# Kernel optimization log

Measured on AMD Instinct MI355X. Metric: run time of the kernel, lower is better.

## Reference

```python
import jax, jax.numpy as jnp
import numpy as np
from jax import lax

B, G, D, S = 1, 2048, 64, 2
H_FULL = 200
H0 = H_FULL // 2 ** (S - 1)
PC_RANGE = (-50.0, -50.0, -4.0, 50.0, 50.0, 4.0)
THRESH = 0.05
CHUNK = 128


def conv3x3(x, w):
    # x: [b,c,h,w], w: [o,i,3,3]
    return lax.conv_general_dilated(x, w, (1, 1), 'SAME',
                                    dimension_numbers=('NCHW', 'OIHW', 'NCHW'))


def instance_norm(x, eps=1e-5):
    mu = x.mean(axis=(2, 3), keepdims=True)
    var = x.var(axis=(2, 3), keepdims=True)
    return (x - mu) / jnp.sqrt(var + eps)


def basic_block(x, w1, w2):
    # conv-(BN@init=identity)-relu-conv-(BN)-add-relu
    h = jax.nn.relu(conv3x3(x, w1))
    h = conv3x3(h, w2)
    return jax.nn.relu(x + h)


def upsampling_add(x, skip, w):
    b, c, h, wd = x.shape
    xu = jax.image.resize(x, (b, c, 2 * h, 2 * wd), method='bilinear')
    xu = instance_norm(conv3x3(xu, w))
    return xu + skip


def render_stage(means, cov6, feats, opac, mask, H, W):
    # Orthographic BEV splatting (3DGS-style EWA + front-to-back compositing).
    g, d = feats.shape
    sh = H / 100.0
    sw = W / 100.0
    # full_proj_transform: px = -sh*y + H/2 ; py = -sw*x + W/2
    u = -sh * means[:, 1] + 0.5 * H
    v = -sw * means[:, 0] + 0.5 * W
    # cov2d = J Sigma J^T + 0.3*I, J = [[0,-sh,0],[-sw,0,0]]
    a = sh * sh * cov6[:, 3] + 0.3
    c = sw * sw * cov6[:, 0] + 0.3
    bb = sh * sw * cov6[:, 1]
    det = jnp.maximum(a * c - bb * bb, 1e-8)
    A = c / det
    Bc = -bb / det
    C = a / det
    xs = jnp.arange(W, dtype=jnp.float32)
    ys = jnp.arange(H, dtype=jnp.float32)
    nc = g // CHUNK

    def step(carry, inp):
        T, out = carry
        u_, v_, A_, B_, C_, op_, mk_, ft_ = inp
        dx = u_[:, None, None] - xs[None, None, :]
        dy = v_[:, None, None] - ys[None, :, None]
        power = (-0.5 * (A_[:, None, None] * dx * dx + C_[:, None, None] * dy * dy)
                 - B_[:, None, None] * dx * dy)
        alpha = jnp.minimum(op_[:, None, None] * jnp.exp(power), 0.99)
        alpha = jnp.where((alpha >= 1.0 / 255.0) & mk_[:, None, None] & (power <= 0.0),
                          alpha, 0.0)
        cp = jnp.cumprod(1.0 - alpha, axis=0)
        t_exc = jnp.concatenate([jnp.ones_like(cp[:1]), cp[:-1]], 0) * T
        out = out + jnp.einsum('ghw,gd->dhw', alpha * t_exc, ft_)
        return (T * cp[-1], out), None

    ch = lambda arr: arr.reshape(nc, CHUNK, *arr.shape[1:])
    init = (jnp.ones((H, W), jnp.float32), jnp.zeros((d, H, W), jnp.float32))
    (_, out), _ = lax.scan(step, init,
                           (ch(u), ch(v), ch(A), ch(Bc), ch(C), ch(opac), ch(mask), ch(feats)))
    return out  # bg color = 0


def setup_inputs() -> dict:
    key = jax.random.key(0)
    ks = jax.random.split(key, 10)
    features = jax.random.normal(ks[0], (B, G, D), jnp.float32)
    xy = jax.random.uniform(ks[1], (B, G, 2), jnp.float32, -55.0, 55.0)
    z = jax.random.uniform(ks[2], (B, G, 1), jnp.float32, -5.0, 5.0)
    means3D = jnp.concatenate([xy, z], -1)
    L = jax.random.normal(ks[3], (B, G, 3, 3), jnp.float32) * 0.5
    Sig = jnp.einsum('bgij,bgkj->bgik', L, L) + 0.1 * jnp.eye(3, dtype=jnp.float32)
    cov3D = jnp.stack([Sig[..., 0, 0], Sig[..., 0, 1], Sig[..., 0, 2],
                       Sig[..., 1, 1], Sig[..., 1, 2], Sig[..., 2, 2]], -1)
    opacities = jax.random.uniform(ks[4], (B, G, S), jnp.float32)
    w_scale = 1.0 / np.sqrt(D * 9)
    bev_emb = jax.random.normal(ks[5], (H0 * H0, D), jnp.float32) * 0.02
    conv1_w = jax.random.normal(ks[6], (S, D, D, 3, 3), jnp.float32) * w_scale
    blk_w = jax.random.normal(ks[7], (S, 2, 2, D, D, 3, 3), jnp.float32) * w_scale
    up_w = jax.random.normal(ks[8], (S - 1, D, D, 3, 3), jnp.float32) * w_scale
    return {'features': features, 'means3D': means3D, 'cov3D': cov3D,
            'opacities': opacities, 'bev_emb': bev_emb, 'conv1_w': conv1_w,
            'blk_w': blk_w, 'up_w': up_w}


def reference(features, means3D, cov3D, opacities, bev_emb, conv1_w, blk_w, up_w):
    b = features.shape[0]
    d = features.shape[-1]
    m = means3D
    mask_pos = ((m[..., 0] >= PC_RANGE[0]) & (m[..., 0] <= PC_RANGE[3]) &
                (m[..., 1] >= PC_RANGE[1]) & (m[..., 1] <= PC_RANGE[4]) &
                (m[..., 2] >= PC_RANGE[2]) & (m[..., 2] <= PC_RANGE[5]))
    num_g = jnp.float32(0.0)
    bevs = []
    for s in range(S):
        H = H0 * 2 ** s
        mask = (opacities[..., s] > THRESH) & mask_pos
        rend = jax.vmap(lambda mn, cv, ft, op, mk: render_stage(mn, cv, ft, op, mk, H, H))
        bevs.append(rend(means3D, cov3D, features, opacities[..., s], mask))
        num_g = num_g + jnp.mean(jnp.sum(mask.astype(jnp.float32), 1))
    x = jnp.broadcast_to(jnp.transpose(bev_emb.reshape(H0, H0, d), (2, 0, 1))[None],
                         (b, d, H0, H0))
    for s in range(S):
        bev = conv3x3(bevs[s], conv1_w[s])
        if s == 0:
            x = x + bev
        else:
            x = upsampling_add(x, bev, up_w[s - 1])
        for blk in range(2):
            x = basic_block(x, blk_w[s, blk, 0], blk_w[s, blk, 1])
    return x, num_g
```

## Files before the change

### kernel.cpp

```cpp
#include <hip/hip_runtime.h>
#include <math.h>

#define G_N 2048
#define CCH 256
#define PSTR 12
#define NBLK 1024
#define WC (64 * 64 * 9)

typedef short bhalf8 __attribute__((ext_vector_type(8)));
typedef float f32x4 __attribute__((ext_vector_type(4)));
typedef unsigned short u16;

__device__ __forceinline__ u16 f2bf(float f) {
    unsigned u = __float_as_uint(f);
    unsigned r = (u + 0x7fffu + ((u >> 16) & 1u)) >> 16;
    return (u16)r;
}
__device__ __forceinline__ float b2f(u16 h) {
    return __uint_as_float((unsigned)h << 16);
}

__device__ __forceinline__ ushort4 chload4(const u16* p) {
    unsigned long long u = __hip_atomic_load((const unsigned long long*)p,
        __ATOMIC_RELAXED, __HIP_MEMORY_SCOPE_AGENT);
    union { unsigned long long u; ushort4 s; } x; x.u = u;
    return x.s;
}
__device__ __forceinline__ void chstore4(u16* p, ushort4 v) {
    union { unsigned long long u; ushort4 s; } x; x.s = v;
    __hip_atomic_store((unsigned long long*)p, x.u,
                       __ATOMIC_RELAXED, __HIP_MEMORY_SCOPE_AGENT);
}
__device__ __forceinline__ float cload(const float* p) {
    return __hip_atomic_load(p, __ATOMIC_RELAXED, __HIP_MEMORY_SCOPE_AGENT);
}

__device__ __forceinline__ void gbar(int* leaf, int* root, int* flag, int phase) {
    asm volatile("s_waitcnt vmcnt(0) lgkmcnt(0)" ::: "memory");
    __syncthreads();
    if (threadIdx.x == 0) {
        int g = blockIdx.x >> 5;
        int old = atomicAdd(&leaf[g * 16], 1);
        if ((old & 31) == 31) {
            int o2 = atomicAdd(root, 1);
            if ((o2 & 31) == 31)
                __hip_atomic_store(flag, phase, __ATOMIC_RELAXED,
                                   __HIP_MEMORY_SCOPE_AGENT);
        }
        while (__hip_atomic_load(flag, __ATOMIC_RELAXED,
                                 __HIP_MEMORY_SCOPE_AGENT) < phase)
            __builtin_amdgcn_s_sleep(4);
    }
    __syncthreads();
    asm volatile("" ::: "memory");
}

__global__ void gls_init(const float* __restrict__ conv1_w,
                         const float* __restrict__ blk_w,
                         const float* __restrict__ up_w,
                         u16* __restrict__ wprep,
                         const float* __restrict__ means,
                         const float* __restrict__ cov6,
                         const float* __restrict__ opac,
                         float* __restrict__ params,
                         int* __restrict__ counts,
                         int* __restrict__ barmem,
                         float* __restrict__ sacc)
{
    int bx = blockIdx.x;
    int tid = threadIdx.x;
    if (bx == 200) {
        for (int i = tid; i < 520; i += 256) barmem[i] = 0;
        if (tid < 128) sacc[tid] = 0.f;
        return;
    }
    if (bx < 198) {
        int p = bx % 18, c = bx / 18;
        const float* src;
        if (c == 0) src = conv1_w;
        else if (c <= 4) src = blk_w + (c - 1) * WC;
        else if (c == 5) src = conv1_w + WC;
        else if (c == 6) src = up_w;
        else src = blk_w + (c - 3) * WC;
        int tap = p >> 1;
        int m = tid >> 6, lane = tid & 63;
        int oc = m * 16 + (lane & 15);
        int ci0 = (p & 1) * 32 + (lane >> 4) * 8;
        u16 v[8];
#pragma unroll
        for (int j = 0; j < 8; ++j)
            v[j] = f2bf(src[(oc * 64 + ci0 + j) * 9 + tap]);
        u16* dst = wprep + ((c * 18 + p) * 4 + m) * 64 * 8 + lane * 8;
#pragma unroll
        for (int j = 0; j < 8; ++j) dst[j] = v[j];
        return;
    }
    int s = bx - 198;
    __shared__ int s_base;
    __shared__ int s_wsum[4];
    if (tid == 0) s_base = 0;
    __syncthreads();
    float* P = params + s * G_N * PSTR;
    float H = (float)(100 << s);
    float sh = (float)(1 << s);
    for (int it = 0; it < G_N / 256; ++it) {
        int g = it * 256 + tid;
        float mx = means[g * 3 + 0], my = means[g * 3 + 1], mz = means[g * 3 + 2];
        float op = opac[g * 2 + s];
        bool mask = (mx >= -50.f && mx <= 50.f && my >= -50.f && my <= 50.f &&
                     mz >= -4.f && mz <= 4.f && op > 0.05f);
        unsigned long long bal = __ballot(mask);
        int lane = tid & 63, wid = tid >> 6;
        int prefix = __popcll(bal & ((1ull << lane) - 1ull));
        if (lane == 0) s_wsum[wid] = __popcll(bal);
        __syncthreads();
        int woff = 0;
        for (int w = 0; w < 4; ++w) if (w < wid) woff += s_wsum[w];
        int pos = s_base + woff + prefix;
        if (mask) {
            float u = -sh * my + 0.5f * H;
            float v = -sh * mx + 0.5f * H;
            float a = sh * sh * cov6[g * 6 + 3] + 0.3f;
            float c = sh * sh * cov6[g * 6 + 0] + 0.3f;
            float bb = sh * sh * cov6[g * 6 + 1];
            float det = fmaxf(a * c - bb * bb, 1e-8f);
            float t = logf(255.f * op);
            float* Q = P + pos * PSTR;
            Q[0] = u; Q[1] = v;
            Q[2] = c / det; Q[3] = -bb / det; Q[4] = a / det;
            Q[5] = op; Q[6] = -t;
            Q[7] = __int_as_float(g);
            Q[8] = sqrtf(2.f * t * a);
            Q[9] = sqrtf(2.f * t * c);
            Q[10] = 0.f; Q[11] = 0.f;
        }
        __syncthreads();
        if (tid == 0) s_base += s_wsum[0] + s_wsum[1] + s_wsum[2] + s_wsum[3];
        __syncthreads();
    }
    if (tid == 0) counts[s] = s_base;
}

__device__ __forceinline__ void render_tile(
    int unit, const float* __restrict__ params, const int* __restrict__ counts,
    const float* __restrict__ feats, u16* __restrict__ out0,
    u16* __restrict__ out1, char* smem)
{
    int s = (unit < 49) ? 0 : 1;
    int t = (s == 0) ? unit : unit - 49;
    int tw = (s == 0) ? 7 : 13;
    int bxx = t % tw, byy = t / tw;
    int H = 100 << s;
    const float* P = params + s * G_N * PSTR;
    u16* out = s ? out1 : out0;
    int cnt = counts[s];

    float* raw = (float*)smem;
    float* cmp = raw + CCH * PSTR;
    int* s_wsum = (int*)(smem + 24576);

    int tid = threadIdx.x;
    int txl = tid & 15, tyl = tid >> 4;
    int px = bxx * 16 + txl;
    int py = byy * 16 + tyl;
    bool active = (px < H) && (py < H);
    float fx = (float)px, fy = (float)py;
    float tx0 = (float)(bxx * 16);
    float tx1 = (float)min(H - 1, bxx * 16 + 15);
    float ty0 = (float)(byy * 16);
    float ty1 = (float)min(H - 1, byy * 16 + 15);

    f32x4 acc[16];
#pragma unroll
    for (int k = 0; k < 16; ++k) acc[k] = (f32x4){0.f, 0.f, 0.f, 0.f};
    float T = 1.f;

    for (int base = 0; base < cnt; base += CCH) {
        int anyalive = __syncthreads_or((int)(active && T > 1e-6f));
        if (!anyalive) break;
        int n = min(CCH, cnt - base);
        for (int i = tid; i < n * 3; i += 256)
            ((float4*)raw)[i] = ((const float4*)(P + base * PSTR))[i];
        __syncthreads();
        bool pass = false;
        if (tid < n) {
            float u = raw[tid * PSTR + 0], v = raw[tid * PSTR + 1];
            float rx = raw[tid * PSTR + 8], ry = raw[tid * PSTR + 9];
            pass = (u + rx >= tx0) && (u - rx <= tx1) &&
                   (v + ry >= ty0) && (v - ry <= ty1);
        }
        unsigned long long bal = __ballot(pass);
        int lane = tid & 63, wid = tid >> 6;
        int prefix = __popcll(bal & ((1ull << lane) - 1ull));
        if (lane == 0) s_wsum[wid] = __popcll(bal);
        __syncthreads();
        int woff = 0;
        for (int w = 0; w < 4; ++w) if (w < wid) woff += s_wsum[w];
        if (pass) {
            float4* dst = (float4*)(cmp + (woff + prefix) * PSTR);
            const float4* src = (const float4*)(raw + tid * PSTR);
            dst[0] = src[0]; dst[1] = src[1]; dst[2] = src[2];
        }
        __syncthreads();
        int nc = s_wsum[0] + s_wsum[1] + s_wsum[2] + s_wsum[3];
        if (active && T > 1e-6f) {
            for (int j = 0; j < nc; ++j) {
                float4 q0 = *(const float4*)(cmp + j * PSTR);
                float4 q1 = *(const float4*)(cmp + j * PSTR + 4);
                float dx = q0.x - fx, dy = q0.y - fy;
                float power = -0.5f * (q0.z * dx * dx + q1.x * dy * dy) - q0.w * dx * dy;
                if (power <= 0.f && power >= q1.z) {
                    float alpha = fminf(q1.y * __expf(power), 0.99f);
                    float wgt = alpha * T;
                    const f32x4* f4 = (const f32x4*)(feats + __float_as_int(q1.w) * 64);
#pragma unroll
                    for (int k = 0; k < 16; ++k) {
                        f32x4 fv = f4[k];
                        acc[k][0] = fmaf(wgt, fv[0], acc[k][0]);
                        acc[k][1] = fmaf(wgt, fv[1], acc[k][1]);
                        acc[k][2] = fmaf(wgt, fv[2], acc[k][2]);
                        acc[k][3] = fmaf(wgt, fv[3], acc[k][3]);
                    }
                    T *= (1.f - alpha);
                }
            }
        }
    }

    float* shf = (float*)smem;
    for (int g = 0; g < 4; ++g) {
        __syncthreads();
        if ((tyl >> 2) == g) {
            int lp = (tyl & 3) * 16 + txl;
#pragma unroll
            for (int k = 0; k < 16; ++k)
                *(float4*)&shf[lp * 68 + 4 * k] =
                    (float4){acc[k][0], acc[k][1], acc[k][2], acc[k][3]};
        }
        __syncthreads();
        for (int j = tid; j < 1024; j += 256) {
            int lp = j >> 4, c4 = (j & 15) * 4;
            int gy = byy * 16 + g * 4 + (lp >> 4);
            int gx = bxx * 16 + (lp & 15);
            if (gy < H && gx < H) {
                float4 v = *(float4*)&shf[lp * 68 + c4];
                ushort4 o = { f2bf(v.x), f2bf(v.y), f2bf(v.z), f2bf(v.w) };
                chstore4(&out[((gy * H + gx) << 6) + c4], o);
            }
        }
    }
}

__device__ __forceinline__ void conv_tile(
    int bx, int H, const u16* __restrict__ in, const u16* __restrict__ wp,
    const float* __restrict__ bev, u16* __restrict__ outb,
    int ups, int dostats, float* __restrict__ sacc, char* smem)
{
    u16* xlds = (u16*)smem;
    u16* fin  = (u16*)(smem + 14400);
    float* red = (float*)(smem + 16384 + 8704);

    int tid = threadIdx.x;
    int gw = (H + 7) >> 3;
    int by = bx / gw, bxx = bx - by * gw;
    int y0 = by * 8, x0 = bxx * 8;
    int w = tid >> 6, lane = tid & 63;
    int n = lane & 15, q = lane >> 4;
    int Hh = H >> 1;
    int oy = (y0 >> 1) - 2, ox = (x0 >> 1) - 2;

    if (ups) {
        for (int i = tid; i < 1024; i += 256) {
            int px = i >> 4, c4 = (i & 15) * 4;
            int iy = px >> 3, ix = px & 7;
            int gyi = oy + iy, gxi = ox + ix;
            ushort4 v = {0, 0, 0, 0};
            if (gyi >= 0 && gyi < Hh && gxi >= 0 && gxi < Hh)
                v = chload4(&in[((gyi * Hh + gxi) << 6) + c4]);
            *(ushort4*)&fin[px * 68 + c4] = v;
        }
        __syncthreads();
    }

    for (int i = tid; i < 1600; i += 256) {
        int px = i >> 4, c4 = (i & 15) * 4;
        int yy = px / 10, xx = px - yy * 10;
        int gy = y0 - 1 + yy, gx = x0 - 1 + xx;
        ushort4 v = {0, 0, 0, 0};
        if (gy >= 0 && gy < H && gx >= 0 && gx < H) {
            if (ups) {
                int yi = gy >> 1, xi = gx >> 1;
                int yb = (gy & 1) ? min(yi + 1, Hh - 1) : max(yi - 1, 0);
                int xb = (gx & 1) ? min(xi + 1, Hh - 1) : max(xi - 1, 0);
                int t0 = yi - oy, t1 = xi - ox, t2 = yb - oy, t3 = xb - ox;
                ushort4 f00 = *(const ushort4*)&fin[(t0 * 8 + t1) * 68 + c4];
                ushort4 f01 = *(const ushort4*)&fin[(t0 * 8 + t3) * 68 + c4];
                ushort4 f10 = *(const ushort4*)&fin[(t2 * 8 + t1) * 68 + c4];
                ushort4 f11 = *(const ushort4*)&fin[(t2 * 8 + t3) * 68 + c4];
                v.x = f2bf(0.5625f * b2f(f00.x) + 0.1875f * (b2f(f01.x) + b2f(f10.x)) + 0.0625f * b2f(f11.x));
                v.y = f2bf(0.5625f * b2f(f00.y) + 0.1875f * (b2f(f01.y) + b2f(f10.y)) + 0.0625f * b2f(f11.y));
                v.z = f2bf(0.5625f * b2f(f00.z) + 0.1875f * (b2f(f01.z) + b2f(f10.z)) + 0.0625f * b2f(f11.z));
                v.w = f2bf(0.5625f * b2f(f00.w) + 0.1875f * (b2f(f01.w) + b2f(f10.w)) + 0.0625f * b2f(f11.w));
            } else {
                v = chload4(&in[((gy * H + gx) << 6) + c4]);
            }
        }
        *(ushort4*)&xlds[px * 72 + c4] = v;
    }
    __syncthreads();

    f32x4 acc[4];
#pragma unroll
    for (int m = 0; m < 4; ++m) acc[m] = (f32x4){0.f, 0.f, 0.f, 0.f};
    const bhalf8* wp8 = (const bhalf8*)wp;
    int sy = 2 * w + (n >> 3), sx = n & 7;

    bhalf8 a0 = wp8[0 * 64 + lane];
    bhalf8 a1 = wp8[1 * 64 + lane];
    bhalf8 a2 = wp8[2 * 64 + lane];
    bhalf8 a3 = wp8[3 * 64 + lane];
    bhalf8 bb = *(const bhalf8*)&xlds[(sy * 10 + sx) * 72 + q * 8];

#pragma unroll 1
    for (int p = 0; p < 18; ++p) {
        bhalf8 na0, na1, na2, na3, nbb;
        if (p < 17) {
            int pn = p + 1;
            na0 = wp8[(pn * 4 + 0) * 64 + lane];
            na1 = wp8[(pn * 4 + 1) * 64 + lane];
            na2 = wp8[(pn * 4 + 2) * 64 + lane];
            na3 = wp8[(pn * 4 + 3) * 64 + lane];
            int tap = pn >> 1, ch = pn & 1;
            int dy = tap / 3, dx = tap - dy * 3;
            nbb = *(const bhalf8*)&xlds[((sy + dy) * 10 + sx + dx) * 72 + ch * 32 + q * 8];
        }
        acc[0] = __builtin_amdgcn_mfma_f32_16x16x32_bf16(a0, bb, acc[0], 0, 0, 0);
        acc[1] = __builtin_amdgcn_mfma_f32_16x16x32_bf16(a1, bb, acc[1], 0, 0, 0);
        acc[2] = __builtin_amdgcn_mfma_f32_16x16x32_bf16(a2, bb, acc[2], 0, 0, 0);
        acc[3] = __builtin_amdgcn_mfma_f32_16x16x32_bf16(a3, bb, acc[3], 0, 0, 0);
        a0 = na0; a1 = na1; a2 = na2; a3 = na3; bb = nbb;
    }

    int gy = y0 + sy, gx = x0 + sx;
    if (gy < H && gx < H) {
        int base = (gy * H + gx) << 6;
#pragma unroll
        for (int m = 0; m < 4; ++m) {
            int oc0 = m * 16 + q * 4;
            float v0 = acc[m][0], v1 = acc[m][1], v2 = acc[m][2], v3 = acc[m][3];
            if (bev) {
                float4 av = *(const float4*)&bev[base + oc0];
                v0 += av.x; v1 += av.y; v2 += av.z; v3 += av.w;
            }
            ushort4 o = { f2bf(v0), f2bf(v1), f2bf(v2), f2bf(v3) };
            chstore4(&outb[base + oc0], o);
        }
    }

    if (dostats) {
#pragma unroll
        for (int m = 0; m < 4; ++m)
#pragma unroll
            for (int r = 0; r < 4; ++r) {
                float v = acc[m][r];
                float s = v, s2 = v * v;
#pragma unroll
                for (int d = 1; d < 16; d <<= 1) {
                    s += __shfl_xor(s, d, 64);
                    s2 += __shfl_xor(s2, d, 64);
                }
                if (n == 0) {
                    int oc = m * 16 + q * 4 + r;
                    red[w * 128 + oc] = s;
                    red[w * 128 + 64 + oc] = s2;
                }
            }
        __syncthreads();
        if (tid < 128) {
            float t = red[tid] + red[128 + tid] + red[256 + tid] + red[384 + tid];
            atomicAdd(&sacc[tid], t);
        }
    }
}

__device__ __forceinline__ void bb_tile(
    int bx, int H, const u16* __restrict__ in,
    const u16* __restrict__ wp1, const u16* __restrict__ wp2,
    u16* __restrict__ outb, float* __restrict__ outf, int final_,
    int nrm, const u16* __restrict__ nskip, const float* __restrict__ sraw,
    char* smem)
{
    u16* xin  = (u16*)smem;
    u16* ilds = (u16*)(smem + 20736);
    float* nm = (float*)(smem + 35136);
    float* nr = nm + 64;

    int tid = threadIdx.x;
    int gw = (H + 7) >> 3;
    int by = bx / gw, bxx = bx - by * gw;
    int y0 = by * 8, x0 = bxx * 8;
    int w = tid >> 6, lane = tid & 63;
    int n = lane & 15, q = lane >> 4;

    if (nrm) {
        if (tid < 64) {
            float s = cload(&sraw[tid]), s2 = cload(&sraw[64 + tid]);
            float mean = s * (1.f / 40000.f);
            float var = s2 * (1.f / 40000.f) - mean * mean;
            nm[tid] = mean;
            nr[tid] = rsqrtf(var + 1e-5f);
        }
        __syncthreads();
    }

    for (int i = tid; i < 2304; i += 256) {
        int px = i >> 4, c4 = (i & 15) * 4;
        int yy = px / 12, xx = px - yy * 12;
        int gy = y0 - 2 + yy, gx = x0 - 2 + xx;
        ushort4 v = {0, 0, 0, 0};
        if (gy >= 0 && gy < H && gx >= 0 && gx < H) {
            int off = ((gy * H + gx) << 6) + c4;
            if (nrm) {
                ushort4 a = chload4(&in[off]);
                ushort4 b = chload4(&nskip[off]);
                v.x = f2bf((b2f(a.x) - nm[c4 + 0]) * nr[c4 + 0] + b2f(b.x));
                v.y = f2bf((b2f(a.y) - nm[c4 + 1]) * nr[c4 + 1] + b2f(b.y));
                v.z = f2bf((b2f(a.z) - nm[c4 + 2]) * nr[c4 + 2] + b2f(b.z));
                v.w = f2bf((b2f(a.w) - nm[c4 + 3]) * nr[c4 + 3] + b2f(b.w));
            } else {
                v = chload4(&in[off]);
            }
        }
        *(ushort4*)&xin[px * 72 + c4] = v;
    }
    __syncthreads();

    const bhalf8* w1 = (const bhalf8*)wp1;
#pragma unroll 1
    for (int r = 0; r < 2; ++r) {
        int t = w + 4 * r;
        int px = t * 16 + n;
        bool val = px < 100;
        int pc = val ? px : 0;
        int yy = pc / 10, xx = pc - yy * 10;

        f32x4 acc[4];
#pragma unroll
        for (int m = 0; m < 4; ++m) acc[m] = (f32x4){0.f, 0.f, 0.f, 0.f};

        bhalf8 a0 = w1[0 * 64 + lane];
        bhalf8 a1 = w1[1 * 64 + lane];
        bhalf8 a2 = w1[2 * 64 + lane];
        bhalf8 a3 = w1[3 * 64 + lane];
        bhalf8 bb = *(const bhalf8*)&xin[(yy * 12 + xx) * 72 + q * 8];

#pragma unroll 1
        for (int p = 0; p < 18; ++p) {
            bhalf8 na0, na1, na2, na3, nbb;
            if (p < 17) {
                int pn = p + 1;
                na0 = w1[(pn * 4 + 0) * 64 + lane];
                na1 = w1[(pn * 4 + 1) * 64 + lane];
                na2 = w1[(pn * 4 + 2) * 64 + lane];
                na3 = w1[(pn * 4 + 3) * 64 + lane];
                int tap = pn >> 1, ch = pn & 1;
                int dy = tap / 3, dx = tap - dy * 3;
                nbb = *(const bhalf8*)&xin[((yy + dy) * 12 + xx + dx) * 72 + ch * 32 + q * 8];
            }
            acc[0] = __builtin_amdgcn_mfma_f32_16x16x32_bf16(a0, bb, acc[0], 0, 0, 0);
            acc[1] = __builtin_amdgcn_mfma_f32_16x16x32_bf16(a1, bb, acc[1], 0, 0, 0);
            acc[2] = __builtin_amdgcn_mfma_f32_16x16x32_bf16(a2, bb, acc[2], 0, 0, 0);
            acc[3] = __builtin_amdgcn_mfma_f32_16x16x32_bf16(a3, bb, acc[3], 0, 0, 0);
            a0 = na0; a1 = na1; a2 = na2; a3 = na3; bb = nbb;
        }

        int iy = y0 - 1 + yy, ix = x0 - 1 + xx;
        bool ok = val && iy >= 0 && iy < H && ix >= 0 && ix < H;
        if (val) {
#pragma unroll
            for (int m = 0; m < 4; ++m) {
                ushort4 o = {0, 0, 0, 0};
                if (ok) {
                    o.x = f2bf(fmaxf(acc[m][0], 0.f));
                    o.y = f2bf(fmaxf(acc[m][1], 0.f));
                    o.z = f2bf(fmaxf(acc[m][2], 0.f));
                    o.w = f2bf(fmaxf(acc[m][3], 0.f));
                }
                *(ushort4*)&ilds[px * 72 + m * 16 + q * 4] = o;
            }
        }
    }
    __syncthreads();

    f32x4 acc[4];
#pragma unroll
    for (int m = 0; m < 4; ++m) acc[m] = (f32x4){0.f, 0.f, 0.f, 0.f};
    const bhalf8* w2 = (const bhalf8*)wp2;
    int sy = 2 * w + (n >> 3), sx = n & 7;

    bhalf8 a0 = w2[0 * 64 + lane];
    bhalf8 a1 = w2[1 * 64 + lane];
    bhalf8 a2 = w2[2 * 64 + lane];
    bhalf8 a3 = w2[3 * 64 + lane];
    bhalf8 bb = *(const bhalf8*)&ilds[(sy * 10 + sx) * 72 + q * 8];

#pragma unroll 1
    for (int p = 0; p < 18; ++p) {
        bhalf8 na0, na1, na2, na3, nbb;
        if (p < 17) {
            int pn = p + 1;
            na0 = w2[(pn * 4 + 0) * 64 + lane];
            na1 = w2[(pn * 4 + 1) * 64 + lane];
            na2 = w2[(pn * 4 + 2) * 64 + lane];
            na3 = w2[(pn * 4 + 3) * 64 + lane];
            int tap = pn >> 1, ch = pn & 1;
            int dy = tap / 3, dx = tap - dy * 3;
            nbb = *(const bhalf8*)&ilds[((sy + dy) * 10 + sx + dx) * 72 + ch * 32 + q * 8];
        }
        acc[0] = __builtin_amdgcn_mfma_f32_16x16x32_bf16(a0, bb, acc[0], 0, 0, 0);
        acc[1] = __builtin_amdgcn_mfma_f32_16x16x32_bf16(a1, bb, acc[1], 0, 0, 0);
        acc[2] = __builtin_amdgcn_mfma_f32_16x16x32_bf16(a2, bb, acc[2], 0, 0, 0);
        acc[3] = __builtin_amdgcn_mfma_f32_16x16x32_bf16(a3, bb, acc[3], 0, 0, 0);
        a0 = na0; a1 = na1; a2 = na2; a3 = na3; bb = nbb;
    }

    int gy = y0 + sy, gx = x0 + sx;
    if (gy < H && gx < H) {
        int base = (gy * H + gx) << 6;
#pragma unroll
        for (int m = 0; m < 4; ++m) {
            int oc0 = m * 16 + q * 4;
            ushort4 xr = *(const ushort4*)&xin[((sy + 2) * 12 + sx + 2) * 72 + oc0];
            float v0 = fmaxf(acc[m][0] + b2f(xr.x), 0.f);
            float v1 = fmaxf(acc[m][1] + b2f(xr.y), 0.f);
            float v2 = fmaxf(acc[m][2] + b2f(xr.z), 0.f);
            float v3 = fmaxf(acc[m][3] + b2f(xr.w), 0.f);
            if (final_) {
                int pix = gy * H + gx;
                outf[(oc0 + 0) * H * H + pix] = v0;
                outf[(oc0 + 1) * H * H + pix] = v1;
                outf[(oc0 + 2) * H * H + pix] = v2;
                outf[(oc0 + 3) * H * H + pix] = v3;
            } else {
                ushort4 o = { f2bf(v0), f2bf(v1), f2bf(v2), f2bf(v3) };
                chstore4(&outb[base + oc0], o);
            }
        }
    }
}

__global__ __launch_bounds__(256, 4) void gls_mega(
    const float* __restrict__ feats, const float* __restrict__ bev_emb,
    const u16* __restrict__ wprep,
    const float* __restrict__ params, const int* __restrict__ cnts,
    u16* __restrict__ R0h, u16* __restrict__ X0h,
    u16* __restrict__ X1h, u16* __restrict__ X2h,
    u16* __restrict__ Qr0h, u16* __restrict__ Sh,
    u16* __restrict__ Uh, u16* __restrict__ Y1h,
    float* __restrict__ out, int* __restrict__ barmem, float* __restrict__ sacc)
{
    __shared__ __align__(16) char smem[36352];
    int bid = blockIdx.x;
    int* leaf = barmem;
    int* root = barmem + 512;
    int* flag = barmem + 513;
    int ph = 0;

    if (bid < 218) render_tile(bid, params, cnts, feats, R0h, Qr0h, smem);
    gbar(leaf, root, flag, ++ph);

    if (bid < 169)
        conv_tile(bid, 100, R0h, wprep + 0 * WC, bev_emb, X0h, 0, 0, nullptr, smem);
    else if (bid < 794)
        conv_tile(bid - 169, 200, Qr0h, wprep + 5 * WC, nullptr, Sh, 0, 0, nullptr, smem);
    gbar(leaf, root, flag, ++ph);

    if (bid < 169)
        bb_tile(bid, 100, X0h, wprep + 1 * WC, wprep + 2 * WC, X1h,
                nullptr, 0, 0, nullptr, nullptr, smem);
    gbar(leaf, root, flag, ++ph);
    if (bid < 169)
        bb_tile(bid, 100, X1h, wprep + 3 * WC, wprep + 4 * WC, X2h,
                nullptr, 0, 0, nullptr, nullptr, smem);
    gbar(leaf, root, flag, ++ph);

    if (bid < 625)
        conv_tile(bid, 200, X2h, wprep + 6 * WC, nullptr, Uh, 1, 1, sacc, smem);
    gbar(leaf, root, flag, ++ph);

    if (bid < 625)
        bb_tile(bid, 200, Uh, wprep + 7 * WC, wprep + 8 * WC, Y1h,
                nullptr, 0, 1, Sh, sacc, smem);
    gbar(leaf, root, flag, ++ph);

    if (bid == 0 && threadIdx.x == 0)
        out[2560000] = (float)(cnts[0] + cnts[1]);
    if (bid < 625)
        bb_tile(bid, 200, Y1h, wprep + 9 * WC, wprep + 10 * WC, nullptr,
                out, 1, 0, nullptr, nullptr, smem);
}

extern "C" void kernel_launch(void* const* d_in, const int* in_sizes, int n_in,
                              void* d_out, int out_size, void* d_ws, size_t ws_size,
                              hipStream_t stream)
{
    const float* feats   = (const float*)d_in[0];
    const float* means   = (const float*)d_in[1];
    const float* cov6    = (const float*)d_in[2];
    const float* opac    = (const float*)d_in[3];
    const float* bev_emb = (const float*)d_in[4];
    const float* conv1_w = (const float*)d_in[5];
    const float* blk_w   = (const float*)d_in[6];
    const float* up_w    = (const float*)d_in[7];
    float* out = (float*)d_out;
    float* ws = (float*)d_ws;

    float* P      = ws;
    int*   cnts   = (int*)(ws + 49152);
    int*   barmem = (int*)(ws + 49280);
    float* sacc   = ws + 49856;
    u16*   wprep  = (u16*)(ws + 50176);

    u16* R0h  = (u16*)(ws + 262144);
    u16* X0h  = (u16*)(ws + 589824);
    u16* X1h  = (u16*)(ws + 917504);
    u16* X2h  = (u16*)(ws + 1245184);
    u16* Qr0h = (u16*)(ws + 1572864);
    u16* Sh   = (u16*)(ws + 2883584);
    u16* Uh   = (u16*)(ws + 4194304);
    u16* Y1h  = (u16*)(ws + 5505024);

    gls_init<<<201, 256, 0, stream>>>(conv1_w, blk_w, up_w, wprep,
                                      means, cov6, opac, P, cnts, barmem, sacc);
    gls_mega<<<NBLK, 256, 0, stream>>>(feats, bev_emb, wprep, P, cnts,
                                       R0h, X0h, X1h, X2h, Qr0h, Sh, Uh, Y1h,
                                       out, barmem, sacc);
    (void)in_sizes; (void)n_in; (void)out_size; (void)ws_size;
}
```

Baseline: 281.7 us.

## Fold init into megakernel and render 8x8 tiles with channel-split waves

Removes the separate init kernel: gaussian compaction runs in two blocks of the persistent kernel before a grid barrier, and weight repacking runs alongside rendering in otherwise idle blocks. Barrier memory is now cleared with a memset. Rendering switches from 16x16 tiles (218 blocks) to 8x8 tiles (794 blocks), where each wave handles 16 of the 64 channels, so register accumulators shrink and more blocks participate. The cost is an extra grid barrier, serial compaction on only two blocks, duplicated culling work across the four waves, and a longer barrier sleep interval.

```diff
diff --git a/kernel.cpp b/kernel.cpp
--- a/kernel.cpp
+++ b/kernel.cpp
@@ -28,6 +28,12 @@
 }
 __device__ __forceinline__ void chstore4(u16* p, ushort4 v) {
     union { unsigned long long u; ushort4 s; } x; x.s = v;
+    __hip_atomic_store((unsigned long long*)p, x.u,
+                       __ATOMIC_RELAXED, __HIP_MEMORY_SCOPE_AGENT);
+}
+__device__ __forceinline__ void cstore8(float* p, float a, float b) {
+    union { unsigned long long u; float f[2]; } x;
+    x.f[0] = a; x.f[1] = b;
     __hip_atomic_store((unsigned long long*)p, x.u,
                        __ATOMIC_RELAXED, __HIP_MEMORY_SCOPE_AGENT);
 }
@@ -49,96 +55,10 @@
         }
         while (__hip_atomic_load(flag, __ATOMIC_RELAXED,
                                  __HIP_MEMORY_SCOPE_AGENT) < phase)
-            __builtin_amdgcn_s_sleep(4);
+            __builtin_amdgcn_s_sleep(16);
     }
     __syncthreads();
     asm volatile("" ::: "memory");
-}
-
-__global__ void gls_init(const float* __restrict__ conv1_w,
-                         const float* __restrict__ blk_w,
-                         const float* __restrict__ up_w,
-                         u16* __restrict__ wprep,
-                         const float* __restrict__ means,
-                         const float* __restrict__ cov6,
-                         const float* __restrict__ opac,
-                         float* __restrict__ params,
-                         int* __restrict__ counts,
-                         int* __restrict__ barmem,
-                         float* __restrict__ sacc)
-{
-    int bx = blockIdx.x;
-    int tid = threadIdx.x;
-    if (bx == 200) {
-        for (int i = tid; i < 520; i += 256) barmem[i] = 0;
-        if (tid < 128) sacc[tid] = 0.f;
-        return;
-    }
-    if (bx < 198) {
-        int p = bx % 18, c = bx / 18;
-        const float* src;
-        if (c == 0) src = conv1_w;
-        else if (c <= 4) src = blk_w + (c - 1) * WC;
-        else if (c == 5) src = conv1_w + WC;
-        else if (c == 6) src = up_w;
-        else src = blk_w + (c - 3) * WC;
-        int tap = p >> 1;
-        int m = tid >> 6, lane = tid & 63;
-        int oc = m * 16 + (lane & 15);
-        int ci0 = (p & 1) * 32 + (lane >> 4) * 8;
-        u16 v[8];
-#pragma unroll
-        for (int j = 0; j < 8; ++j)
-            v[j] = f2bf(src[(oc * 64 + ci0 + j) * 9 + tap]);
-        u16* dst = wprep + ((c * 18 + p) * 4 + m) * 64 * 8 + lane * 8;
-#pragma unroll
-        for (int j = 0; j < 8; ++j) dst[j] = v[j];
-        return;
-    }
-    int s = bx - 198;
-    __shared__ int s_base;
-    __shared__ int s_wsum[4];
-    if (tid == 0) s_base = 0;
-    __syncthreads();
-    float* P = params + s * G_N * PSTR;
-    float H = (float)(100 << s);
-    float sh = (float)(1 << s);
-    for (int it = 0; it < G_N / 256; ++it) {
-        int g = it * 256 + tid;
-        float mx = means[g * 3 + 0], my = means[g * 3 + 1], mz = means[g * 3 + 2];
-        float op = opac[g * 2 + s];
-        bool mask = (mx >= -50.f && mx <= 50.f && my >= -50.f && my <= 50.f &&
-                     mz >= -4.f && mz <= 4.f && op > 0.05f);
-        unsigned long long bal = __ballot(mask);
-        int lane = tid & 63, wid = tid >> 6;
-        int prefix = __popcll(bal & ((1ull << lane) - 1ull));
-        if (lane == 0) s_wsum[wid] = __popcll(bal);
-        __syncthreads();
-        int woff = 0;
-        for (int w = 0; w < 4; ++w) if (w < wid) woff += s_wsum[w];
-        int pos = s_base + woff + prefix;
-        if (mask) {
-            float u = -sh * my + 0.5f * H;
-            float v = -sh * mx + 0.5f * H;
-            float a = sh * sh * cov6[g * 6 + 3] + 0.3f;
-            float c = sh * sh * cov6[g * 6 + 0] + 0.3f;
-            float bb = sh * sh * cov6[g * 6 + 1];
-            float det = fmaxf(a * c - bb * bb, 1e-8f);
-            float t = logf(255.f * op);
-            float* Q = P + pos * PSTR;
-            Q[0] = u; Q[1] = v;
-            Q[2] = c / det; Q[3] = -bb / det; Q[4] = a / det;
-            Q[5] = op; Q[6] = -t;
-            Q[7] = __int_as_float(g);
-            Q[8] = sqrtf(2.f * t * a);
-            Q[9] = sqrtf(2.f * t * c);
-            Q[10] = 0.f; Q[11] = 0.f;
-        }
-        __syncthreads();
-        if (tid == 0) s_base += s_wsum[0] + s_wsum[1] + s_wsum[2] + s_wsum[3];
-        __syncthreads();
-    }
-    if (tid == 0) counts[s] = s_base;
 }
 
 __device__ __forceinline__ void render_tile(
@@ -146,9 +66,9 @@
     const float* __restrict__ feats, u16* __restrict__ out0,
     u16* __restrict__ out1, char* smem)
 {
-    int s = (unit < 49) ? 0 : 1;
-    int t = (s == 0) ? unit : unit - 49;
-    int tw = (s == 0) ? 7 : 13;
+    int s = (unit < 169) ? 0 : 1;
+    int t = (s == 0) ? unit : unit - 169;
+    int tw = (s == 0) ? 13 : 25;
     int bxx = t % tw, byy = t / tw;
     int H = 100 << s;
     const float* P = params + s * G_N * PSTR;
@@ -160,19 +80,18 @@
     int* s_wsum = (int*)(smem + 24576);
 
     int tid = threadIdx.x;
-    int txl = tid & 15, tyl = tid >> 4;
-    int px = bxx * 16 + txl;
-    int py = byy * 16 + tyl;
+    int w = tid >> 6, lane = tid & 63;
+    int pxl = lane & 7, pyl = lane >> 3;
+    int x0 = bxx * 8, y0 = byy * 8;
+    int px = x0 + pxl, py = y0 + pyl;
     bool active = (px < H) && (py < H);
     float fx = (float)px, fy = (float)py;
-    float tx0 = (float)(bxx * 16);
-    float tx1 = (float)min(H - 1, bxx * 16 + 15);
-    float ty0 = (float)(byy * 16);
-    float ty1 = (float)min(H - 1, byy * 16 + 15);
-
-    f32x4 acc[16];
-#pragma unroll
-    for (int k = 0; k < 16; ++k) acc[k] = (f32x4){0.f, 0.f, 0.f, 0.f};
+    float tx0 = (float)x0, tx1 = (float)min(H - 1, x0 + 7);
+    float ty0 = (float)y0, ty1 = (float)min(H - 1, y0 + 7);
+
+    f32x4 acc[4];
+#pragma unroll
+    for (int k = 0; k < 4; ++k) acc[k] = (f32x4){0.f, 0.f, 0.f, 0.f};
     float T = 1.f;
 
     for (int base = 0; base < cnt; base += CCH) {
@@ -190,12 +109,11 @@
                    (v + ry >= ty0) && (v - ry <= ty1);
         }
         unsigned long long bal = __ballot(pass);
-        int lane = tid & 63, wid = tid >> 6;
         int prefix = __popcll(bal & ((1ull << lane) - 1ull));
-        if (lane == 0) s_wsum[wid] = __popcll(bal);
+        if (lane == 0) s_wsum[w] = __popcll(bal);
         __syncthreads();
         int woff = 0;
-        for (int w = 0; w < 4; ++w) if (w < wid) woff += s_wsum[w];
+        for (int k = 0; k < 4; ++k) if (k < w) woff += s_wsum[k];
         if (pass) {
             float4* dst = (float4*)(cmp + (woff + prefix) * PSTR);
             const float4* src = (const float4*)(raw + tid * PSTR);
@@ -212,9 +130,9 @@
                 if (power <= 0.f && power >= q1.z) {
                     float alpha = fminf(q1.y * __expf(power), 0.99f);
                     float wgt = alpha * T;
-                    const f32x4* f4 = (const f32x4*)(feats + __float_as_int(q1.w) * 64);
-#pragma unroll
-                    for (int k = 0; k < 16; ++k) {
+                    const f32x4* f4 = (const f32x4*)(feats + __float_as_int(q1.w) * 64) + w * 4;
+#pragma unroll
+                    for (int k = 0; k < 4; ++k) {
                         f32x4 fv = f4[k];
                         acc[k][0] = fmaf(wgt, fv[0], acc[k][0]);
                         acc[k][1] = fmaf(wgt, fv[1], acc[k][1]);
@@ -227,26 +145,20 @@
         }
     }
 
+    __syncthreads();
     float* shf = (float*)smem;
-    for (int g = 0; g < 4; ++g) {
-        __syncthreads();
-        if ((tyl >> 2) == g) {
-            int lp = (tyl & 3) * 16 + txl;
-#pragma unroll
-            for (int k = 0; k < 16; ++k)
-                *(float4*)&shf[lp * 68 + 4 * k] =
-                    (float4){acc[k][0], acc[k][1], acc[k][2], acc[k][3]};
-        }
-        __syncthreads();
-        for (int j = tid; j < 1024; j += 256) {
-            int lp = j >> 4, c4 = (j & 15) * 4;
-            int gy = byy * 16 + g * 4 + (lp >> 4);
-            int gx = bxx * 16 + (lp & 15);
-            if (gy < H && gx < H) {
-                float4 v = *(float4*)&shf[lp * 68 + c4];
-                ushort4 o = { f2bf(v.x), f2bf(v.y), f2bf(v.z), f2bf(v.w) };
-                chstore4(&out[((gy * H + gx) << 6) + c4], o);
-            }
+#pragma unroll
+    for (int k = 0; k < 4; ++k)
+        *(float4*)&shf[lane * 68 + w * 16 + k * 4] =
+            (float4){acc[k][0], acc[k][1], acc[k][2], acc[k][3]};
+    __syncthreads();
+    for (int j = tid; j < 1024; j += 256) {
+        int lp = j >> 4, c4 = (j & 15) * 4;
+        int gy = y0 + (lp >> 3), gx = x0 + (lp & 7);
+        if (gy < H && gx < H) {
+            float4 v = *(float4*)&shf[lp * 68 + c4];
+            ushort4 o = { f2bf(v.x), f2bf(v.y), f2bf(v.z), f2bf(v.w) };
+            chstore4(&out[((gy * H + gx) << 6) + c4], o);
         }
     }
 }
@@ -551,8 +463,10 @@
 
 __global__ __launch_bounds__(256, 4) void gls_mega(
     const float* __restrict__ feats, const float* __restrict__ bev_emb,
-    const u16* __restrict__ wprep,
-    const float* __restrict__ params, const int* __restrict__ cnts,
+    const float* __restrict__ conv1_w, const float* __restrict__ blk_w,
+    const float* __restrict__ up_w, const float* __restrict__ means,
+    const float* __restrict__ cov6, const float* __restrict__ opac,
+    u16* __restrict__ wprep, float* __restrict__ params, int* __restrict__ cnts,
     u16* __restrict__ R0h, u16* __restrict__ X0h,
     u16* __restrict__ X1h, u16* __restrict__ X2h,
     u16* __restrict__ Qr0h, u16* __restrict__ Sh,
@@ -561,12 +475,83 @@
 {
     __shared__ __align__(16) char smem[36352];
     int bid = blockIdx.x;
+    int tid = threadIdx.x;
     int* leaf = barmem;
     int* root = barmem + 512;
     int* flag = barmem + 513;
     int ph = 0;
 
-    if (bid < 218) render_tile(bid, params, cnts, feats, R0h, Qr0h, smem);
+    if (bid < 2) {
+        int s = bid;
+        int* s_base = (int*)smem;
+        int* s_wsum = s_base + 16;
+        if (tid == 0) *s_base = 0;
+        __syncthreads();
+        float* P = params + s * G_N * PSTR;
+        float H = (float)(100 << s);
+        float sh = (float)(1 << s);
+        for (int it = 0; it < G_N / 256; ++it) {
+            int g = it * 256 + tid;
+            float mx = means[g * 3 + 0], my = means[g * 3 + 1], mz = means[g * 3 + 2];
+            float op = opac[g * 2 + s];
+            bool mask = (mx >= -50.f && mx <= 50.f && my >= -50.f && my <= 50.f &&
+                         mz >= -4.f && mz <= 4.f && op > 0.05f);
+            unsigned long long bal = __ballot(mask);
+            int lane = tid & 63, wid = tid >> 6;
+            int prefix = __popcll(bal & ((1ull << lane) - 1ull));
+            if (lane == 0) s_wsum[wid] = __popcll(bal);
+            __syncthreads();
+            int woff = 0;
+            for (int w = 0; w < 4; ++w) if (w < wid) woff += s_wsum[w];
+            int pos = *s_base + woff + prefix;
+            if (mask) {
+                float u = -sh * my + 0.5f * H;
+                float v = -sh * mx + 0.5f * H;
+                float a = sh * sh * cov6[g * 6 + 3] + 0.3f;
+                float c = sh * sh * cov6[g * 6 + 0] + 0.3f;
+                float bb = sh * sh * cov6[g * 6 + 1];
+                float det = fmaxf(a * c - bb * bb, 1e-8f);
+                float t = logf(255.f * op);
+                float* Q = P + pos * PSTR;
+                cstore8(&Q[0], u, v);
+                cstore8(&Q[2], c / det, -bb / det);
+                cstore8(&Q[4], a / det, op);
+                cstore8(&Q[6], -t, __int_as_float(g));
+                cstore8(&Q[8], sqrtf(2.f * t * a), sqrtf(2.f * t * c));
+            }
+            __syncthreads();
+            if (tid == 0) *s_base += s_wsum[0] + s_wsum[1] + s_wsum[2] + s_wsum[3];
+            __syncthreads();
+        }
+        if (tid == 0)
+            __hip_atomic_store(&cnts[s], *s_base, __ATOMIC_RELAXED,
+                               __HIP_MEMORY_SCOPE_AGENT);
+    }
+    gbar(leaf, root, flag, ++ph);
+
+    if (bid < 794) {
+        render_tile(bid, params, cnts, feats, R0h, Qr0h, smem);
+    } else if (bid < 992) {
+        int rb = bid - 794;
+        int p = rb % 18, c = rb / 18;
+        const float* src;
+        if (c == 0) src = conv1_w;
+        else if (c <= 4) src = blk_w + (c - 1) * WC;
+        else if (c == 5) src = conv1_w + WC;
+        else if (c == 6) src = up_w;
+        else src = blk_w + (c - 3) * WC;
+        int tap = p >> 1;
+        int m = tid >> 6, lane = tid & 63;
+        int oc = m * 16 + (lane & 15);
+        int ci0 = (p & 1) * 32 + (lane >> 4) * 8;
+        u16 v[8];
+#pragma unroll
+        for (int j = 0; j < 8; ++j)
+            v[j] = f2bf(src[(oc * 64 + ci0 + j) * 9 + tap]);
+        u16* dst = wprep + ((c * 18 + p) * 4 + m) * 64 * 8 + lane * 8;
+        chstore4(dst, (ushort4){v[0], v[1], v[2], v[3]});
+        chstore4(dst + 4, (ushort4){v[4], v[5], v[6], v[7]});
+    }
     gbar(leaf, root, flag, ++ph);
 
     if (bid < 169)
@@ -630,9 +615,9 @@
     u16* Uh   = (u16*)(ws + 4194304);
     u16* Y1h  = (u16*)(ws + 5505024);
 
-    gls_init<<<201, 256, 0, stream>>>(conv1_w, blk_w, up_w, wprep,
-                                      means, cov6, opac, P, cnts, barmem, sacc);
-    gls_mega<<<NBLK, 256, 0, stream>>>(feats, bev_emb, wprep, P, cnts,
+    hipMemsetAsync(barmem, 0, (520 + 64 + 128) * 4, stream);
+    gls_mega<<<NBLK, 256, 0, stream>>>(feats, bev_emb, conv1_w, blk_w, up_w,
+                                       means, cov6, opac, wprep, P, cnts,
                                        R0h, X0h, X1h, X2h, Qr0h, Sh, Uh, Y1h,
                                        out, barmem, sacc);
     (void)in_sizes; (void)n_in; (void)out_size; (void)ws_size;
```

Measured after the change: 269.2 us. 4.5% less time.
